# Kernel optimization log

Measured on AMD Instinct MI355X. Metric: run time of the kernel, lower is better.

Reference implementation:

```python
import jax, jax.numpy as jnp
import numpy as np

ALPHA = 0.2  # LeakyReLU negative slope
N_NODES = 8192
IN_F = 512
OUT_F = 64


def setup_inputs() -> dict:
    key = jax.random.key(0)
    k1, k2, k3, k4, k5 = jax.random.split(key, 5)
    x = jax.random.normal(k1, (N_NODES, IN_F), dtype=jnp.float32)
    n = jax.random.normal(k2, (N_NODES, IN_F), dtype=jnp.float32)
    # nn.Linear default init scale ~ 1/sqrt(fan_in)
    W_tran = jax.random.normal(k3, (OUT_F, IN_F), dtype=jnp.float32) / np.sqrt(IN_F)
    w_att1 = jax.random.normal(k4, (OUT_F,), dtype=jnp.float32) / np.sqrt(OUT_F)
    w_att2 = jax.random.normal(k5, (OUT_F,), dtype=jnp.float32) / np.sqrt(OUT_F)
    return {"x": x, "n": n, "W_tran": W_tran, "w_att1": w_att1, "w_att2": w_att2}


def reference(x, n, W_tran, w_att1, w_att2):
    # h1: [N, out], h2: [N, out]
    h1 = x @ W_tran.T
    h2 = n @ W_tran.T
    # additive attention scores: a[i, j] = att1(h1)_i + att2(h2)_j  -> [N, N]
    s1 = h1 @ w_att1  # [N]
    s2 = h2 @ w_att2  # [N]
    a = s1[:, None] + s2[None, :]
    a = jnp.where(a >= 0, a, ALPHA * a)  # LeakyReLU
    attn = jax.nn.softmax(a, axis=1)     # Softmax(dim=1) over keys
    return attn @ h1  # [N, out]
```

## Files before the change

### kernel.cpp

```cpp
#include <hip/hip_runtime.h>
#include <math.h>

#define NN    8192
#define KF    512
#define DF    64
#define NCH   32
#define EC    136

__global__ __launch_bounds__(256) void k_main(const float* __restrict__ x,
        const float* __restrict__ nmat, const float* __restrict__ W,
        const float* __restrict__ w1, const float* __restrict__ w2,
        float* __restrict__ h1, float* __restrict__ s1, float* __restrict__ s2) {
    const int tid = threadIdx.x;
    if (blockIdx.x < 128) {
        __shared__ float xs[32][68];
        __shared__ float wt[32][64];
        const int row0 = blockIdx.x * 64;
        const int ty = tid >> 4, tx = tid & 15;
        const int sr = tid >> 3;
        const int sc = (tid & 7) * 4;
        const int wd = tid & 63;
        const int wg = tid >> 6;
        float4 xv0 = *reinterpret_cast<const float4*>(x + (size_t)(row0 + sr) * KF + sc);
        float4 xv1 = *reinterpret_cast<const float4*>(x + (size_t)(row0 + 32 + sr) * KF + sc);
        float4 wv0 = *reinterpret_cast<const float4*>(W + (size_t)wd * KF + wg * 8);
        float4 wv1 = *reinterpret_cast<const float4*>(W + (size_t)wd * KF + wg * 8 + 4);
        float acc[4][4] = {};
        for (int kc = 0; kc < 16; ++kc) {
            __syncthreads();
            xs[sc+0][sr]=xv0.x; xs[sc+1][sr]=xv0.y; xs[sc+2][sr]=xv0.z; xs[sc+3][sr]=xv0.w;
            xs[sc+0][32+sr]=xv1.x; xs[sc+1][32+sr]=xv1.y; xs[sc+2][32+sr]=xv1.z; xs[sc+3][32+sr]=xv1.w;
            wt[wg*8+0][wd]=wv0.x; wt[wg*8+1][wd]=wv0.y; wt[wg*8+2][wd]=wv0.z; wt[wg*8+3][wd]=wv0.w;
            wt[wg*8+4][wd]=wv1.x; wt[wg*8+5][wd]=wv1.y; wt[wg*8+6][wd]=wv1.z; wt[wg*8+7][wd]=wv1.w;
            __syncthreads();
            if (kc < 15) {
                const int kk = (kc + 1) * 32;
                xv0 = *reinterpret_cast<const float4*>(x + (size_t)(row0 + sr) * KF + kk + sc);
                xv1 = *reinterpret_cast<const float4*>(x + (size_t)(row0 + 32 + sr) * KF + kk + sc);
                wv0 = *reinterpret_cast<const float4*>(W + (size_t)wd * KF + kk + wg * 8);
                wv1 = *reinterpret_cast<const float4*>(W + (size_t)wd * KF + kk + wg * 8 + 4);
            }
            #pragma unroll
            for (int k = 0; k < 32; ++k) {
                const float4 a4 = *reinterpret_cast<const float4*>(&xs[k][ty * 4]);
                const float4 b4 = *reinterpret_cast<const float4*>(&wt[k][tx * 4]);
                const float av[4] = {a4.x, a4.y, a4.z, a4.w};
                const float bv[4] = {b4.x, b4.y, b4.z, b4.w};
                #pragma unroll
                for (int i = 0; i < 4; ++i)
                    #pragma unroll
                    for (int j = 0; j < 4; ++j)
                        acc[i][j] = fmaf(av[i], bv[j], acc[i][j]);
            }
        }
        const float4 wv = *reinterpret_cast<const float4*>(w1 + tx * 4);
        #pragma unroll
        for (int i = 0; i < 4; ++i) {
            const int r = row0 + ty * 4 + i;
            *reinterpret_cast<float4*>(h1 + (size_t)r * DF + tx * 4) =
                make_float4(acc[i][0], acc[i][1], acc[i][2], acc[i][3]);
            float p = acc[i][0] * wv.x + acc[i][1] * wv.y + acc[i][2] * wv.z + acc[i][3] * wv.w;
            #pragma unroll
            for (int off = 1; off < 16; off <<= 1) p += __shfl_xor(p, off);
            if (tx == 0) s1[r] = p;
        }
    } else {
        __shared__ float v2s[KF];
        const int row0 = (blockIdx.x - 128) * 32;
        float a0 = 0.f, a1 = 0.f;
        for (int d = 0; d < DF; ++d) {
            const float wd2 = w2[d];
            a0 = fmaf(W[(size_t)d * KF + tid],       wd2, a0);
            a1 = fmaf(W[(size_t)d * KF + 256 + tid], wd2, a1);
        }
        v2s[tid] = a0; v2s[tid + 256] = a1;
        __syncthreads();
        const int lane = tid & 63, w = tid >> 6;
        const float4 b0 = *reinterpret_cast<const float4*>(&v2s[lane * 4]);
        const float4 b1 = *reinterpret_cast<const float4*>(&v2s[256 + lane * 4]);
        for (int rr = 0; rr < 8; ++rr) {
            const int row = row0 + w * 8 + rr;
            const float4 n0 = *reinterpret_cast<const float4*>(nmat + (size_t)row * KF + lane * 4);
            const float4 n1 = *reinterpret_cast<const float4*>(nmat + (size_t)row * KF + 256 + lane * 4);
            float acc = n0.x * b0.x;
            acc = fmaf(n0.y, b0.y, acc); acc = fmaf(n0.z, b0.z, acc); acc = fmaf(n0.w, b0.w, acc);
            acc = fmaf(n1.x, b1.x, acc); acc = fmaf(n1.y, b1.y, acc);
            acc = fmaf(n1.z, b1.z, acc); acc = fmaf(n1.w, b1.w, acc);
            #pragma unroll
            for (int off = 32; off; off >>= 1) acc += __shfl_xor(acc, off);
            if (lane == 0) s2[row] = acc;
        }
    }
}

__device__ __forceinline__ unsigned int f2key(float f) {
    unsigned int u = __float_as_uint(f);
    return u ^ ((u >> 31) ? 0xFFFFFFFFu : 0x80000000u);
}

__global__ __launch_bounds__(256) void k_rank(const float* __restrict__ s2,
        int* __restrict__ order, float* __restrict__ s2s,
        double* __restrict__ wpos, double* __restrict__ wneg) {
    __shared__ unsigned int sk[NN];
    __shared__ int part[256];
    const int tid = threadIdx.x;
    {
        const float4* src = reinterpret_cast<const float4*>(s2);
        #pragma unroll
        for (int t = 0; t < 8; ++t) {
            const float4 v = src[tid + t * 256];
            const int b = (tid + t * 256) * 4;
            sk[b] = f2key(v.x); sk[b+1] = f2key(v.y); sk[b+2] = f2key(v.z); sk[b+3] = f2key(v.w);
        }
    }
    __syncthreads();
    const int jl = tid & 15, seg = tid >> 4;
    const int j = blockIdx.x * 16 + jl;
    const unsigned int mk = sk[j];
    const int base = seg * 512;
    int cnt = 0;
    for (int q = 0; q < 128; ++q) {
        const int e = (q * 4 + seg * 4) & 511;
        const int idx = base + e;
        const uint4 v = *reinterpret_cast<const uint4*>(&sk[idx]);
        cnt += (v.x < mk) | ((v.x == mk) & (idx     < j));
        cnt += (v.y < mk) | ((v.y == mk) & (idx + 1 < j));
        cnt += (v.z < mk) | ((v.z == mk) & (idx + 2 < j));
        cnt += (v.w < mk) | ((v.w == mk) & (idx + 3 < j));
    }
    part[tid] = cnt;
    __syncthreads();
    if (tid < 16) {
        int r = 0;
        #pragma unroll
        for (int s = 0; s < 16; ++s) r += part[s * 16 + tid];
        const int jj = blockIdx.x * 16 + tid;
        const float v = s2[jj];
        order[r] = jj;
        s2s[r] = v;
        wpos[r] = exp((double)v);
        wneg[r] = exp(0.2 * (double)v);
    }
}

__device__ __forceinline__ void load_vals(int g, int p, const float* __restrict__ h1,
        const int* __restrict__ order, const double* __restrict__ wpos,
        const double* __restrict__ wneg, double* vals, int& ncols, int& colbase) {
    if (g < 16) {
        ncols = 8;
        const int d0 = (g < 8) ? 8 * g : 8 * (g - 8);
        colbase = (g < 8) ? d0 : 64 + d0;
        const double wgt = (g < 8) ? wpos[p] : wneg[p];
        const float* hp = h1 + (size_t)order[p] * DF + d0;
        const float4 h0 = *reinterpret_cast<const float4*>(hp);
        const float4 h4 = *reinterpret_cast<const float4*>(hp + 4);
        vals[0]=wgt*h0.x; vals[1]=wgt*h0.y; vals[2]=wgt*h0.z; vals[3]=wgt*h0.w;
        vals[4]=wgt*h4.x; vals[5]=wgt*h4.y; vals[6]=wgt*h4.z; vals[7]=wgt*h4.w;
    } else {
        ncols = 2; colbase = 128;
        vals[0] = wpos[p]; vals[1] = wneg[p];
    }
}

__global__ __launch_bounds__(256) void k_csum(const float* __restrict__ h1,
        const int* __restrict__ order, const double* __restrict__ wpos,
        const double* __restrict__ wneg, double* __restrict__ cT) {
    const int g = blockIdx.x, c = blockIdx.y;
    const int tid = threadIdx.x, lane = tid & 63, w = tid >> 6;
    const int p = c * 256 + tid;
    double vals[8]; int ncols, colbase;
    load_vals(g, p, h1, order, wpos, wneg, vals, ncols, colbase);
    __shared__ double red[4][8];
    for (int jj = 0; jj < ncols; ++jj) {
        double r = vals[jj];
        #pragma unroll
        for (int off = 32; off; off >>= 1) r += __shfl_xor(r, off);
        if (lane == 0) red[w][jj] = r;
    }
    __syncthreads();
    if (tid < ncols)
        cT[(size_t)(colbase + tid) * NCH + c] = red[0][tid] + red[1][tid] + red[2][tid] + red[3][tid];
}

__global__ __launch_bounds__(256) void k_scan(const float* __restrict__ h1,
        const int* __restrict__ order, const double* __restrict__ wpos,
        const double* __restrict__ wneg, const double* __restrict__ cT,
        double* __restrict__ E) {
    const int g = blockIdx.x, c = blockIdx.y;
    const int tid = threadIdx.x, lane = tid & 63, w = tid >> 6;
    const int p = c * 256 + tid;
    double vals[8], inc8[8]; int ncols, colbase;
    load_vals(g, p, h1, order, wpos, wneg, vals, ncols, colbase);
    __shared__ double cOs[8];
    __shared__ double wtot[4][8];
    if (tid < ncols) {
        double s = 0.0;
        const double* ct = cT + (size_t)(colbase + tid) * NCH;
        for (int cc = 0; cc < c; ++cc) s += ct[cc];
        cOs[tid] = s;
    }
    for (int jj = 0; jj < ncols; ++jj) {
        double incl = vals[jj];
        #pragma unroll
        for (int off = 1; off < 64; off <<= 1) {
            double t = __shfl_up(incl, off);
            if (lane >= off) incl += t;
        }
        inc8[jj] = incl;
        if (lane == 63) wtot[w][jj] = incl;
    }
    __syncthreads();
    double* Ep = E + (size_t)p * EC + colbase;
    for (int jj = 0; jj < ncols; ++jj) {
        double woff = cOs[jj];
        for (int ww = 0; ww < w; ++ww) woff += wtot[ww][jj];
        Ep[jj] = woff + inc8[jj] - vals[jj];
    }
    if (c == NCH - 1 && tid < ncols)
        E[(size_t)NN * EC + colbase + tid] =
            cOs[tid] + wtot[0][tid] + wtot[1][tid] + wtot[2][tid] + wtot[3][tid];
}

__global__ __launch_bounds__(256) void k_out(const float* __restrict__ s1,
        const float* __restrict__ s2s, const double* __restrict__ E,
        float* __restrict__ out) {
    const int lane = threadIdx.x & 63, wave = threadIdx.x >> 6;
    const int i = blockIdx.x * 4 + wave;
    const float s1v = s1[i];
    const float t = -s1v;
    int lo = 0, hi = NN;
    while (lo < hi) {
        int mid = (lo + hi) >> 1;
        if (s2s[mid] < t) lo = mid + 1; else hi = mid;
    }
    const double* Ek = E + (size_t)lo * EC;
    const double* Et = E + (size_t)NN * EC;
    const double e1 = exp((double)s1v);
    const double e2 = exp(0.2 * (double)s1v);
    const double num = e1 * (Et[lane] - Ek[lane]) + e2 * Ek[64 + lane];
    const double den = e1 * (Et[128] - Ek[128]) + e2 * Ek[129];
    out[(size_t)i * DF + lane] = (float)(num / den);
}

extern "C" void kernel_launch(void* const* d_in, const int* in_sizes, int n_in,
                              void* d_out, int out_size, void* d_ws, size_t ws_size,
                              hipStream_t stream) {
    const float* x    = (const float*)d_in[0];
    const float* nmat = (const float*)d_in[1];
    const float* W    = (const float*)d_in[2];
    const float* w1   = (const float*)d_in[3];
    const float* w2   = (const float*)d_in[4];
    float* out = (float*)d_out;

    char* ws = (char*)d_ws;
    size_t off = 0;
    auto alloc = [&](size_t bytes) -> void* {
        void* p = ws + off;
        off += (bytes + 255) & ~(size_t)255;
        return p;
    };
    float*  h1    = (float*)alloc((size_t)NN * DF * 4);
    float*  s1    = (float*)alloc((size_t)NN * 4);
    float*  s2    = (float*)alloc((size_t)NN * 4);
    int*    order = (int*)alloc((size_t)NN * 4);
    float*  s2s   = (float*)alloc((size_t)NN * 4);
    double* wpos  = (double*)alloc((size_t)NN * 8);
    double* wneg  = (double*)alloc((size_t)NN * 8);
    double* cT    = (double*)alloc((size_t)130 * NCH * 8);
    double* E     = (double*)alloc((size_t)(NN + 1) * EC * 8);

    k_main<<<384, 256, 0, stream>>>(x, nmat, W, w1, w2, h1, s1, s2);
    k_rank<<<512, 256, 0, stream>>>(s2, order, s2s, wpos, wneg);
    k_csum<<<dim3(17, NCH), 256, 0, stream>>>(h1, order, wpos, wneg, cT);
    k_scan<<<dim3(17, NCH), 256, 0, stream>>>(h1, order, wpos, wneg, cT, E);
    k_out<<<NN / 4, 256, 0, stream>>>(s1, s2s, E, out);
}
```

Before: 87.05 us.

## Restructure projection GEMM, rank two keys per thread, batch output binary searches

The h1 projection now gives each lane one row and 8 output columns. It stages a 64x128 swizzled tile of x in shared memory and reads W directly from global/cache, with two blocks per row tile. The s1 reduction moves out of k_main into k_out, which recomputes it from h1. k_out also stages sorted s2 in LDS and runs four interleaved binary searches per wave. k_rank handles two keys per thread to halve the shared-memory scans per comparison. These changes target LDS traffic and latency in several kernels, at the cost of heavier global W reads in the GEMM and extra h1 reads in k_out.

```diff
diff --git a/kernel.cpp b/kernel.cpp
--- a/kernel.cpp
+++ b/kernel.cpp
@@ -9,64 +9,58 @@
 
 __global__ __launch_bounds__(256) void k_main(const float* __restrict__ x,
         const float* __restrict__ nmat, const float* __restrict__ W,
-        const float* __restrict__ w1, const float* __restrict__ w2,
-        float* __restrict__ h1, float* __restrict__ s1, float* __restrict__ s2) {
+        const float* __restrict__ w2,
+        float* __restrict__ h1, float* __restrict__ s2) {
+    __shared__ float xs[64 * 128];
     const int tid = threadIdx.x;
-    if (blockIdx.x < 128) {
-        __shared__ float xs[32][68];
-        __shared__ float wt[32][64];
-        const int row0 = blockIdx.x * 64;
-        const int ty = tid >> 4, tx = tid & 15;
-        const int sr = tid >> 3;
-        const int sc = (tid & 7) * 4;
-        const int wd = tid & 63;
-        const int wg = tid >> 6;
-        float4 xv0 = *reinterpret_cast<const float4*>(x + (size_t)(row0 + sr) * KF + sc);
-        float4 xv1 = *reinterpret_cast<const float4*>(x + (size_t)(row0 + 32 + sr) * KF + sc);
-        float4 wv0 = *reinterpret_cast<const float4*>(W + (size_t)wd * KF + wg * 8);
-        float4 wv1 = *reinterpret_cast<const float4*>(W + (size_t)wd * KF + wg * 8 + 4);
-        float acc[4][4] = {};
-        for (int kc = 0; kc < 16; ++kc) {
+    if (blockIdx.x < 256) {
+        const int row0 = (blockIdx.x >> 1) * 64;
+        const int c0   = (blockIdx.x & 1) * 32;
+        const int l = tid & 63;
+        const int w = __builtin_amdgcn_readfirstlane(tid >> 6);
+        const int d0 = c0 + w * 8;
+        float acc[8] = {};
+        float4 pf[8];
+        #pragma unroll
+        for (int q = 0; q < 8; ++q) {
+            const int idx = q * 256 + tid, r = idx >> 5, c4 = (idx & 31) * 4;
+            pf[q] = *reinterpret_cast<const float4*>(x + (size_t)(row0 + r) * KF + c4);
+        }
+        for (int kc = 0; kc < 4; ++kc) {
             __syncthreads();
-            xs[sc+0][sr]=xv0.x; xs[sc+1][sr]=xv0.y; xs[sc+2][sr]=xv0.z; xs[sc+3][sr]=xv0.w;
-            xs[sc+0][32+sr]=xv1.x; xs[sc+1][32+sr]=xv1.y; xs[sc+2][32+sr]=xv1.z; xs[sc+3][32+sr]=xv1.w;
-            wt[wg*8+0][wd]=wv0.x; wt[wg*8+1][wd]=wv0.y; wt[wg*8+2][wd]=wv0.z; wt[wg*8+3][wd]=wv0.w;
-            wt[wg*8+4][wd]=wv1.x; wt[wg*8+5][wd]=wv1.y; wt[wg*8+6][wd]=wv1.z; wt[wg*8+7][wd]=wv1.w;
+            #pragma unroll
+            for (int q = 0; q < 8; ++q) {
+                const int idx = q * 256 + tid, r = idx >> 5, c4 = (idx & 31) * 4;
+                *reinterpret_cast<float4*>(&xs[r * 128 + (c4 ^ ((r & 7) << 2))]) = pf[q];
+            }
             __syncthreads();
-            if (kc < 15) {
-                const int kk = (kc + 1) * 32;
-                xv0 = *reinterpret_cast<const float4*>(x + (size_t)(row0 + sr) * KF + kk + sc);
-                xv1 = *reinterpret_cast<const float4*>(x + (size_t)(row0 + 32 + sr) * KF + kk + sc);
-                wv0 = *reinterpret_cast<const float4*>(W + (size_t)wd * KF + kk + wg * 8);
-                wv1 = *reinterpret_cast<const float4*>(W + (size_t)wd * KF + kk + wg * 8 + 4);
+            if (kc < 3) {
+                #pragma unroll
+                for (int q = 0; q < 8; ++q) {
+                    const int idx = q * 256 + tid, r = idx >> 5, c4 = (idx & 31) * 4;
+                    pf[q] = *reinterpret_cast<const float4*>(
+                        x + (size_t)(row0 + r) * KF + (kc + 1) * 128 + c4);
+                }
             }
-            #pragma unroll
-            for (int k = 0; k < 32; ++k) {
-                const float4 a4 = *reinterpret_cast<const float4*>(&xs[k][ty * 4]);
-                const float4 b4 = *reinterpret_cast<const float4*>(&wt[k][tx * 4]);
-                const float av[4] = {a4.x, a4.y, a4.z, a4.w};
-                const float bv[4] = {b4.x, b4.y, b4.z, b4.w};
+            const float* Wb = W + (size_t)d0 * KF + kc * 128;
+            #pragma unroll 4
+            for (int q = 0; q < 32; ++q) {
+                const float4 a = *reinterpret_cast<const float4*>(
+                    &xs[l * 128 + ((q * 4) ^ ((l & 7) << 2))]);
                 #pragma unroll
-                for (int i = 0; i < 4; ++i)
-                    #pragma unroll
-                    for (int j = 0; j < 4; ++j)
-                        acc[i][j] = fmaf(av[i], bv[j], acc[i][j]);
+                for (int j = 0; j < 8; ++j) {
+                    const float4 b = *reinterpret_cast<const float4*>(Wb + (size_t)j * KF + q * 4);
+                    acc[j] = fmaf(a.x, b.x, fmaf(a.y, b.y, fmaf(a.z, b.z, fmaf(a.w, b.w, acc[j]))));
+                }
             }
         }
-        const float4 wv = *reinterpret_cast<const float4*>(w1 + tx * 4);
-        #pragma unroll
-        for (int i = 0; i < 4; ++i) {
-            const int r = row0 + ty * 4 + i;
-            *reinterpret_cast<float4*>(h1 + (size_t)r * DF + tx * 4) =
-                make_float4(acc[i][0], acc[i][1], acc[i][2], acc[i][3]);
-            float p = acc[i][0] * wv.x + acc[i][1] * wv.y + acc[i][2] * wv.z + acc[i][3] * wv.w;
-            #pragma unroll
-            for (int off = 1; off < 16; off <<= 1) p += __shfl_xor(p, off);
-            if (tx == 0) s1[r] = p;
-        }
+        *reinterpret_cast<float4*>(h1 + (size_t)(row0 + l) * DF + d0) =
+            make_float4(acc[0], acc[1], acc[2], acc[3]);
+        *reinterpret_cast<float4*>(h1 + (size_t)(row0 + l) * DF + d0 + 4) =
+            make_float4(acc[4], acc[5], acc[6], acc[7]);
     } else {
-        __shared__ float v2s[KF];
-        const int row0 = (blockIdx.x - 128) * 32;
+        float* v2s = xs;
+        const int row0 = (int)(blockIdx.x - 256) * 32;
         float a0 = 0.f, a1 = 0.f;
         for (int d = 0; d < DF; ++d) {
             const float wd2 = w2[d];
@@ -102,7 +96,7 @@
         int* __restrict__ order, float* __restrict__ s2s,
         double* __restrict__ wpos, double* __restrict__ wneg) {
     __shared__ unsigned int sk[NN];
-    __shared__ int part[256];
+    __shared__ int2 part[8][32];
     const int tid = threadIdx.x;
     {
         const float4* src = reinterpret_cast<const float4*>(s2);
@@ -114,27 +108,32 @@
         }
     }
     __syncthreads();
-    const int jl = tid & 15, seg = tid >> 4;
-    const int j = blockIdx.x * 16 + jl;
-    const unsigned int mk = sk[j];
-    const int base = seg * 512;
-    int cnt = 0;
-    for (int q = 0; q < 128; ++q) {
-        const int e = (q * 4 + seg * 4) & 511;
-        const int idx = base + e;
+    const int jl = tid & 7, seg = tid >> 3;
+    const int j0 = blockIdx.x * 16 + jl, j1 = j0 + 8;
+    const unsigned int k0 = sk[j0], k1 = sk[j1];
+    const int base = seg * 256;
+    int c0 = 0, c1 = 0;
+    for (int q = 0; q < 64; ++q) {
+        const int qq = (q + seg) & 63;
+        const int idx = base + qq * 4;
         const uint4 v = *reinterpret_cast<const uint4*>(&sk[idx]);
-        cnt += (v.x < mk) | ((v.x == mk) & (idx     < j));
-        cnt += (v.y < mk) | ((v.y == mk) & (idx + 1 < j));
-        cnt += (v.z < mk) | ((v.z == mk) & (idx + 2 < j));
-        cnt += (v.w < mk) | ((v.w == mk) & (idx + 3 < j));
-    }
-    part[tid] = cnt;
+        c0 += (v.x < k0) | ((v.x == k0) & (idx     < j0));
+        c0 += (v.y < k0) | ((v.y == k0) & (idx + 1 < j0));
+        c0 += (v.z < k0) | ((v.z == k0) & (idx + 2 < j0));
+        c0 += (v.w < k0) | ((v.w == k0) & (idx + 3 < j0));
+        c1 += (v.x < k1) | ((v.x == k1) & (idx     < j1));
+        c1 += (v.y < k1) | ((v.y == k1) & (idx + 1 < j1));
+        c1 += (v.z < k1) | ((v.z == k1) & (idx + 2 < j1));
+        c1 += (v.w < k1) | ((v.w == k1) & (idx + 3 < j1));
+    }
+    part[jl][seg] = make_int2(c0, c1);
     __syncthreads();
     if (tid < 16) {
+        const int jloc = tid & 7, hi = tid >> 3;
         int r = 0;
         #pragma unroll
-        for (int s = 0; s < 16; ++s) r += part[s * 16 + tid];
-        const int jj = blockIdx.x * 16 + tid;
+        for (int s = 0; s < 32; ++s) r += hi ? part[jloc][s].y : part[jloc][s].x;
+        const int jj = blockIdx.x * 16 + jloc + 8 * hi;
         const float v = s2[jj];
         order[r] = jj;
         s2s[r] = v;
@@ -221,25 +220,47 @@
             cOs[tid] + wtot[0][tid] + wtot[1][tid] + wtot[2][tid] + wtot[3][tid];
 }
 
-__global__ __launch_bounds__(256) void k_out(const float* __restrict__ s1,
-        const float* __restrict__ s2s, const double* __restrict__ E,
-        float* __restrict__ out) {
-    const int lane = threadIdx.x & 63, wave = threadIdx.x >> 6;
-    const int i = blockIdx.x * 4 + wave;
-    const float s1v = s1[i];
-    const float t = -s1v;
-    int lo = 0, hi = NN;
-    while (lo < hi) {
-        int mid = (lo + hi) >> 1;
-        if (s2s[mid] < t) lo = mid + 1; else hi = mid;
-    }
-    const double* Ek = E + (size_t)lo * EC;
+__global__ __launch_bounds__(256) void k_out(const float* __restrict__ h1,
+        const float* __restrict__ w1, const float* __restrict__ s2s,
+        const double* __restrict__ E, float* __restrict__ out) {
+    __shared__ float ss[NN];
+    const int tid = threadIdx.x;
+    {
+        const float4* src = reinterpret_cast<const float4*>(s2s);
+        float4* dst = reinterpret_cast<float4*>(ss);
+        #pragma unroll
+        for (int t = 0; t < 8; ++t) dst[tid + t * 256] = src[tid + t * 256];
+    }
+    __syncthreads();
+    const int lane = tid & 63, w = tid >> 6;
+    const int i0 = blockIdx.x * 16 + w * 4;
+    const float wl = w1[lane];
+    float s1v[4];
+    #pragma unroll
+    for (int r = 0; r < 4; ++r) {
+        float p = h1[(size_t)(i0 + r) * DF + lane] * wl;
+        #pragma unroll
+        for (int off = 32; off; off >>= 1) p += __shfl_xor(p, off);
+        s1v[r] = p;
+    }
+    int lo[4] = {0, 0, 0, 0}, hi[4] = {NN, NN, NN, NN};
+    for (int step = 0; step < 13; ++step) {
+        #pragma unroll
+        for (int r = 0; r < 4; ++r) {
+            const int mid = (lo[r] + hi[r]) >> 1;
+            if (ss[mid] < -s1v[r]) lo[r] = mid + 1; else hi[r] = mid;
+        }
+    }
     const double* Et = E + (size_t)NN * EC;
-    const double e1 = exp((double)s1v);
-    const double e2 = exp(0.2 * (double)s1v);
-    const double num = e1 * (Et[lane] - Ek[lane]) + e2 * Ek[64 + lane];
-    const double den = e1 * (Et[128] - Ek[128]) + e2 * Ek[129];
-    out[(size_t)i * DF + lane] = (float)(num / den);
+    #pragma unroll
+    for (int r = 0; r < 4; ++r) {
+        const double* Ek = E + (size_t)lo[r] * EC;
+        const double e1 = exp((double)s1v[r]);
+        const double e2 = exp(0.2 * (double)s1v[r]);
+        const double num = e1 * (Et[lane] - Ek[lane]) + e2 * Ek[64 + lane];
+        const double den = e1 * (Et[128] - Ek[128]) + e2 * Ek[129];
+        out[(size_t)(i0 + r) * DF + lane] = (float)(num / den);
+    }
 }
 
 extern "C" void kernel_launch(void* const* d_in, const int* in_sizes, int n_in,
@@ -260,7 +281,6 @@
         return p;
     };
     float*  h1    = (float*)alloc((size_t)NN * DF * 4);
-    float*  s1    = (float*)alloc((size_t)NN * 4);
     float*  s2    = (float*)alloc((size_t)NN * 4);
     int*    order = (int*)alloc((size_t)NN * 4);
     float*  s2s   = (float*)alloc((size_t)NN * 4);
@@ -269,9 +289,9 @@
     double* cT    = (double*)alloc((size_t)130 * NCH * 8);
     double* E     = (double*)alloc((size_t)(NN + 1) * EC * 8);
 
-    k_main<<<384, 256, 0, stream>>>(x, nmat, W, w1, w2, h1, s1, s2);
+    k_main<<<512, 256, 0, stream>>>(x, nmat, W, w2, h1, s2);
     k_rank<<<512, 256, 0, stream>>>(s2, order, s2s, wpos, wneg);
     k_csum<<<dim3(17, NCH), 256, 0, stream>>>(h1, order, wpos, wneg, cT);
     k_scan<<<dim3(17, NCH), 256, 0, stream>>>(h1, order, wpos, wneg, cT, E);
-    k_out<<<NN / 4, 256, 0, stream>>>(s1, s2s, E, out);
-}
+    k_out<<<NN / 16, 256, 0, stream>>>(h1, w1, s2s, E, out);
+}
```

Result: slower. 119.7 us (+37.5%).
